# Optimization experiments

Measured on AMD Instinct MI355X. Metric: run time of the kernel, lower is better.

Reference implementation:

```python
import jax, jax.numpy as jnp
import numpy as np

N_NODES = 100000
N_EDGES = 1600000
IN_FEATS = 64
N_HIDDEN = 64
OUT_FEATS = 64


def setup_inputs() -> dict:
    key = jax.random.key(0)
    ks = jax.random.split(key, 12)
    feat = jax.random.normal(ks[0], (N_NODES, IN_FEATS), dtype=jnp.float32)
    # per-node symmetric degree normalization coefficients (e.g. 1/sqrt(deg))
    norm_data = jax.random.uniform(ks[1], (N_NODES,), dtype=jnp.float32, minval=0.1, maxval=1.0)
    src = jax.random.randint(ks[2], (N_EDGES,), 0, N_NODES)
    dst = jax.random.randint(ks[3], (N_EDGES,), 0, N_NODES)
    s = 0.05
    return {
        "feat": feat,
        "norm_data": norm_data,
        "src": src,
        "dst": dst,
        "W0": jax.random.normal(ks[4], (IN_FEATS, N_HIDDEN), dtype=jnp.float32) * s,
        "b0": jnp.zeros((N_HIDDEN,), dtype=jnp.float32),
        "W1": jax.random.normal(ks[5], (N_HIDDEN, N_HIDDEN), dtype=jnp.float32) * s,
        "b1": jnp.zeros((N_HIDDEN,), dtype=jnp.float32),
        "W2": jax.random.normal(ks[6], (N_HIDDEN, OUT_FEATS), dtype=jnp.float32) * s,
        "b2": jnp.zeros((OUT_FEATS,), dtype=jnp.float32),
    }


def _graph_conv(h, norm, src, dst, W, b, activation):
    # DGL GraphConv, norm='both': scale by src norm, project, aggregate over
    # edges (gather at src, scatter-add at dst), scale by dst norm, add bias.
    h = h * norm[:, None]                 # [N, d_in]
    h = h @ W                             # project first (d_in <= d_out path)
    msgs = jnp.take(h, src, axis=0)       # [E, d_out] irregular gather
    agg = jax.ops.segment_sum(msgs, dst, num_segments=N_NODES)  # [N, d_out]
    h = agg * norm[:, None] + b
    return jax.nn.relu(h) if activation else h


def reference(feat, norm_data, src, dst, W0, b0, W1, b1, W2, b2):
    h = _graph_conv(feat, norm_data, src, dst, W0, b0, True)
    h = _graph_conv(h, norm_data, src, dst, W1, b1, True)
    h = _graph_conv(h, norm_data, src, dst, W2, b2, False)
    return h
```

## Files before the change

kernel.cpp:

```cpp
#include <hip/hip_runtime.h>

#define FEATS 64
#define BTILE 32
#define MAX_NB 3200
#define CH 8192
#define SORT_CAP 2048
#define NPW 8

__device__ __forceinline__ float bf2f(unsigned short b) {
    unsigned u = (unsigned)b << 16;
    float f; __builtin_memcpy(&f, &u, 4); return f;
}
__device__ __forceinline__ unsigned short f2bf(float f) {
    unsigned u; __builtin_memcpy(&u, &f, 4);
    u += 0x7FFFu + ((u >> 16) & 1u);
    return (unsigned short)(u >> 16);
}
__device__ __forceinline__ float lo16(unsigned u) {
    unsigned v = u << 16; float f; __builtin_memcpy(&f, &v, 4); return f;
}
__device__ __forceinline__ float hi16(unsigned u) {
    unsigned v = u & 0xFFFF0000u; float f; __builtin_memcpy(&f, &v, 4); return f;
}

__global__ __launch_bounds__(256) void scale_kernel(
    const float* __restrict__ feat, const float* __restrict__ norm,
    unsigned short* __restrict__ out, int n4) {
    const int i = blockIdx.x * 256 + threadIdx.x;
    if (i >= n4) return;
    float4 v = reinterpret_cast<const float4*>(feat)[i];
    const float nv = norm[i >> 4];
    uint2 p;
    p.x = (unsigned)f2bf(v.x * nv) | ((unsigned)f2bf(v.y * nv) << 16);
    p.y = (unsigned)f2bf(v.z * nv) | ((unsigned)f2bf(v.w * nv) << 16);
    reinterpret_cast<uint2*>(out)[i] = p;
}

__global__ __launch_bounds__(1024) void hist_pass(
    const int* __restrict__ dst, int* __restrict__ hist, int E, int NB) {
    __shared__ int lh[MAX_NB];
    for (int i = threadIdx.x; i < NB; i += 1024) lh[i] = 0;
    __syncthreads();
    const int k  = blockIdx.x;
    const int e0 = k * CH, e1 = min(E, e0 + CH);
    for (int e = e0 + threadIdx.x; e < e1; e += 1024)
        atomicAdd(&lh[dst[e] >> 5], 1);
    __syncthreads();
    for (int b = threadIdx.x; b < NB; b += 1024)
        hist[(size_t)k * NB + b] = lh[b];
}

__global__ __launch_bounds__(256) void bucket_scan(
    int* hist, int* __restrict__ btotal, int NB, int NCHUNK) {
    __shared__ int sa[256], sb[256];
    const int b = blockIdx.x, t = threadIdx.x;
    const int v = (t < NCHUNK) ? hist[(size_t)t * NB + b] : 0;
    sa[t] = v;
    __syncthreads();
    int *cur = sa, *nxt = sb;
    for (int off = 1; off < 256; off <<= 1) {
        nxt[t] = cur[t] + ((t >= off) ? cur[t - off] : 0);
        __syncthreads();
        int* tmp = cur; cur = nxt; nxt = tmp;
    }
    if (t < NCHUNK) hist[(size_t)t * NB + b] = cur[t] - v;
    if (t == 255) btotal[b] = cur[255];
}

__global__ __launch_bounds__(1024) void base_scan(
    const int* __restrict__ btotal, int* __restrict__ bstart, int NB, int E) {
    __shared__ int sa[1024], sb[1024];
    __shared__ int carry;
    const int t = threadIdx.x;
    if (t == 0) carry = 0;
    __syncthreads();
    for (int base = 0; base < NB; base += 1024) {
        const int i = base + t;
        const int v = (i < NB) ? btotal[i] : 0;
        sa[t] = v;
        __syncthreads();
        int *cur = sa, *nxt = sb;
        for (int off = 1; off < 1024; off <<= 1) {
            nxt[t] = cur[t] + ((t >= off) ? cur[t - off] : 0);
            __syncthreads();
            int* tmp = cur; cur = nxt; nxt = tmp;
        }
        const int c = carry;
        if (i < NB) bstart[i] = c + cur[t] - v;
        __syncthreads();
        if (t == 1023) carry = c + cur[1023];
        __syncthreads();
    }
    if (t == 0) bstart[NB] = E;
}

__global__ __launch_bounds__(1024) void scatter_pack(
    const int* __restrict__ src, const int* __restrict__ dst,
    const int* __restrict__ prebase, const int* __restrict__ bstart,
    unsigned int* __restrict__ packed, int E, int NB) {
    __shared__ int cur[MAX_NB];
    const int k = blockIdx.x;
    for (int b = threadIdx.x; b < NB; b += 1024)
        cur[b] = bstart[b] + prebase[(size_t)k * NB + b];
    __syncthreads();
    const int e0 = k * CH, e1 = min(E, e0 + CH);
    for (int e = e0 + threadIdx.x; e < e1; e += 1024) {
        const int d = dst[e];
        const int p = atomicAdd(&cur[d >> 5], 1);
        packed[p] = ((unsigned)(d & 31) << 26) | (unsigned)src[e];
    }
}

__global__ __launch_bounds__(256) void sort_bucket(
    unsigned int* packed, const int* __restrict__ bstart,
    int* __restrict__ rowptr, int NB, int E) {
    __shared__ unsigned ent[SORT_CAP];
    __shared__ int cnt[BTILE];
    __shared__ int base[BTILE];
    const int b = blockIdx.x;
    const int beg = bstart[b], end = bstart[b + 1];
    const int n = end - beg;
    const int t = threadIdx.x;
    if (t < BTILE) cnt[t] = 0;
    __syncthreads();
    if (n <= SORT_CAP) {
        for (int i = t; i < n; i += 256) {
            const unsigned v = packed[beg + i];
            ent[i] = v;
            atomicAdd(&cnt[v >> 26], 1);
        }
    } else {
        for (int i = t; i < n; i += 256) atomicAdd(&cnt[packed[beg + i] >> 26], 1);
    }
    __syncthreads();
    if (t == 0) {
        int run = 0;
        for (int i = 0; i < BTILE; ++i) {
            const int c = cnt[i]; base[i] = run; cnt[i] = run; run += c;
        }
    }
    __syncthreads();
    if (t < BTILE) rowptr[b * BTILE + t] = beg + base[t];
    if (b == NB - 1 && t == 0) rowptr[NB * BTILE] = E;
    if (n <= SORT_CAP) {
        for (int i = t; i < n; i += 256) {
            const unsigned v = ent[i];
            const int p = atomicAdd(&cnt[v >> 26], 1);
            packed[beg + p] = v;
        }
    }
}

#define ACC8(d, m) do { \
    a0 = fmaf(lo16((d).x), (m), a0); a1 = fmaf(hi16((d).x), (m), a1); \
    a2 = fmaf(lo16((d).y), (m), a2); a3 = fmaf(hi16((d).y), (m), a3); \
    a4 = fmaf(lo16((d).z), (m), a4); a5 = fmaf(hi16((d).z), (m), a5); \
    a6 = fmaf(lo16((d).w), (m), a6); a7 = fmaf(hi16((d).w), (m), a7); } while (0)

#define RED(off) do { \
    a0 += __shfl_xor(a0, off, 64); a1 += __shfl_xor(a1, off, 64); \
    a2 += __shfl_xor(a2, off, 64); a3 += __shfl_xor(a3, off, 64); \
    a4 += __shfl_xor(a4, off, 64); a5 += __shfl_xor(a5, off, 64); \
    a6 += __shfl_xor(a6, off, 64); a7 += __shfl_xor(a7, off, 64); } while (0)

__device__ __forceinline__ uint4 row16(const unsigned short* hs, unsigned pk, int chunk) {
    return *((const uint4*)((const char*)hs + (size_t)(pk & 0x3FFFFFFu) * 128) + chunk);
}

__global__ __launch_bounds__(64, 4) void agg_proj(
    const unsigned int* __restrict__ packed, const int* __restrict__ rowptr,
    const unsigned short* __restrict__ hs, const float* __restrict__ norm,
    const float* __restrict__ W, const float* __restrict__ bias,
    void* __restrict__ outv, int N, int E, int mode) {
    __shared__ float accs[NPW * FEATS];
    const int lane  = threadIdx.x & 63;
    const int slot  = lane >> 3;
    const int chunk = lane & 7;
    const int node0 = blockIdx.x * NPW;

    int rbv[NPW], rev[NPW];
    unsigned c[NPW];
#pragma unroll
    for (int i = 0; i < NPW; ++i) {
        const int node = node0 + i;
        const int cl = node < N ? node : N - 1;
        rbv[i] = rowptr[cl];
        rev[i] = (node < N) ? rowptr[cl + 1] : rbv[i];
        c[i]   = packed[min(rbv[i] + lane, E - 1)];
    }

#pragma unroll
    for (int i = 0; i < NPW; ++i) {
        float a0 = 0.f, a1 = 0.f, a2 = 0.f, a3 = 0.f,
              a4 = 0.f, a5 = 0.f, a6 = 0.f, a7 = 0.f;
        const int deg = rev[i] - rbv[i];
        if (deg > 0) {
            const int segn = min(deg, 64);
            const int no   = (segn + 7) >> 3;
            unsigned pk = (unsigned)__builtin_amdgcn_ds_bpermute(slot << 2, (int)c[i]);
            uint4 d = row16(hs, pk, chunk);
            float m = (slot < segn) ? 1.f : 0.f;
            for (int o = 1; o < no; ++o) {
                const int idx = o * 8 + slot;
                unsigned pk1 = (unsigned)__builtin_amdgcn_ds_bpermute(idx << 2, (int)c[i]);
                uint4 d1 = row16(hs, pk1, chunk);
                ACC8(d, m);
                d = d1; m = (idx < segn) ? 1.f : 0.f;
            }
            ACC8(d, m);
            for (int p = rbv[i] + 64; p < rev[i]; p += 64) {
                const int sn = min(rev[i] - p, 64);
                const unsigned cw2 = packed[min(p + lane, E - 1)];
                const int no2 = (sn + 7) >> 3;
                for (int o = 0; o < no2; ++o) {
                    const int idx = o * 8 + slot;
                    unsigned pk2 = (unsigned)__builtin_amdgcn_ds_bpermute(idx << 2, (int)cw2);
                    uint4 d2 = row16(hs, pk2, chunk);
                    const float m2 = (idx < sn) ? 1.f : 0.f;
                    ACC8(d2, m2);
                }
            }
        }
        RED(8); RED(16); RED(32);
        if (slot == 0) {
            float4* dstp = (float4*)&accs[i * FEATS + chunk * 8];
            dstp[0] = make_float4(a0, a1, a2, a3);
            dstp[1] = make_float4(a4, a5, a6, a7);
        }
    }
    __syncthreads();

    float s[NPW];
#pragma unroll
    for (int i = 0; i < NPW; ++i) s[i] = 0.f;
#pragma unroll 1
    for (int k4 = 0; k4 < 16; ++k4) {
        const float w0 = W[(4 * k4 + 0) * FEATS + lane];
        const float w1 = W[(4 * k4 + 1) * FEATS + lane];
        const float w2 = W[(4 * k4 + 2) * FEATS + lane];
        const float w3 = W[(4 * k4 + 3) * FEATS + lane];
#pragma unroll
        for (int i = 0; i < NPW; ++i) {
            const float4 a = *(const float4*)&accs[i * FEATS + 4 * k4];
            s[i] = fmaf(a.w, w3, fmaf(a.z, w2, fmaf(a.y, w1, fmaf(a.x, w0, s[i]))));
        }
    }
    const float bi = bias[lane];
#pragma unroll
    for (int i = 0; i < NPW; ++i) {
        const int node = node0 + i;
        if (node >= N) break;
        const float nv = norm[node];
        float o = fmaf(s[i], nv, bi);
        if (mode) {
            o = fmaxf(o, 0.f) * nv;
            ((unsigned short*)outv)[(size_t)node * FEATS + lane] = f2bf(o);
        } else {
            ((float*)outv)[(size_t)node * FEATS + lane] = o;
        }
    }
}

extern "C" void kernel_launch(void* const* d_in, const int* in_sizes, int n_in,
                              void* d_out, int out_size, void* d_ws, size_t ws_size,
                              hipStream_t stream) {
    const float* feat = (const float*)d_in[0];
    const float* norm = (const float*)d_in[1];
    const int*   src  = (const int*)d_in[2];
    const int*   dst  = (const int*)d_in[3];
    const float* W0   = (const float*)d_in[4];
    const float* b0   = (const float*)d_in[5];
    const float* W1   = (const float*)d_in[6];
    const float* b1   = (const float*)d_in[7];
    const float* W2   = (const float*)d_in[8];
    const float* b2   = (const float*)d_in[9];

    float* out = (float*)d_out;
    const int N = in_sizes[0] / FEATS;
    const int E = in_sizes[2];
    const int NB = (N + BTILE - 1) / BTILE;
    const int NCHUNK = (E + CH - 1) / CH;

    unsigned short* H0 = (unsigned short*)d_ws;
    unsigned short* H1 = H0 + (size_t)N * FEATS;
    unsigned* packed = (unsigned*)(H1 + (size_t)N * FEATS);
    int*      hist   = (int*)(packed + E);
    int*      btotal = hist + (size_t)NCHUNK * NB;
    int*      bstart = btotal + NB;
    int*      rowptr = bstart + NB + 1;

    hist_pass<<<NCHUNK, 1024, 0, stream>>>(dst, hist, E, NB);
    bucket_scan<<<NB, 256, 0, stream>>>(hist, btotal, NB, NCHUNK);
    base_scan<<<1, 1024, 0, stream>>>(btotal, bstart, NB, E);
    scatter_pack<<<NCHUNK, 1024, 0, stream>>>(src, dst, hist, bstart, packed, E, NB);
    sort_bucket<<<NB, 256, 0, stream>>>(packed, bstart, rowptr, NB, E);

    const int agrid = (N + NPW - 1) / NPW;
    const int sgrid = (N * 16 + 255) / 256;

    scale_kernel<<<sgrid, 256, 0, stream>>>(feat, norm, H0, N * 16);

    agg_proj<<<agrid, 64, 0, stream>>>(packed, rowptr, H0, norm, W0, b0, H1, N, E, 1);
    agg_proj<<<agrid, 64, 0, stream>>>(packed, rowptr, H1, norm, W1, b1, H0, N, E, 1);
    agg_proj<<<agrid, 64, 0, stream>>>(packed, rowptr, H0, norm, W2, b2, out, N, E, 0);
}
```

Measured before the change: 221.0 us.

## Assign each 8-lane group to one node instead of whole wave per node

Restructures the aggregation so each group of 8 lanes owns one destination node and walks its neighbour list sequentially, instead of the whole 64-lane wave cooperatively gathering one node's edges and reducing across lanes with shuffles. This removes the bpermute broadcasts, the masked FMAs and the cross-lane shuffle reductions, and gives per-node parallelism across the eight nodes in a block. In exchange, each lane group serially loads one packed index per edge with a short prefetch, so latency hiding per node is lower and degree imbalance among the eight nodes causes divergence within the wave.

```diff
diff --git a/kernel.cpp b/kernel.cpp
--- a/kernel.cpp
+++ b/kernel.cpp
@@ -151,17 +151,11 @@
     }
 }
 
-#define ACC8(d, m) do { \
-    a0 = fmaf(lo16((d).x), (m), a0); a1 = fmaf(hi16((d).x), (m), a1); \
-    a2 = fmaf(lo16((d).y), (m), a2); a3 = fmaf(hi16((d).y), (m), a3); \
-    a4 = fmaf(lo16((d).z), (m), a4); a5 = fmaf(hi16((d).z), (m), a5); \
-    a6 = fmaf(lo16((d).w), (m), a6); a7 = fmaf(hi16((d).w), (m), a7); } while (0)
-
-#define RED(off) do { \
-    a0 += __shfl_xor(a0, off, 64); a1 += __shfl_xor(a1, off, 64); \
-    a2 += __shfl_xor(a2, off, 64); a3 += __shfl_xor(a3, off, 64); \
-    a4 += __shfl_xor(a4, off, 64); a5 += __shfl_xor(a5, off, 64); \
-    a6 += __shfl_xor(a6, off, 64); a7 += __shfl_xor(a7, off, 64); } while (0)
+#define ADD8(d) do { \
+    a0 += lo16((d).x); a1 += hi16((d).x); \
+    a2 += lo16((d).y); a3 += hi16((d).y); \
+    a4 += lo16((d).z); a5 += hi16((d).z); \
+    a6 += lo16((d).w); a7 += hi16((d).w); } while (0)
 
 __device__ __forceinline__ uint4 row16(const unsigned short* hs, unsigned pk, int chunk) {
     return *((const uint4*)((const char*)hs + (size_t)(pk & 0x3FFFFFFu) * 128) + chunk);
@@ -177,56 +171,31 @@
     const int slot  = lane >> 3;
     const int chunk = lane & 7;
     const int node0 = blockIdx.x * NPW;
-
-    int rbv[NPW], rev[NPW];
-    unsigned c[NPW];
-#pragma unroll
-    for (int i = 0; i < NPW; ++i) {
-        const int node = node0 + i;
-        const int cl = node < N ? node : N - 1;
-        rbv[i] = rowptr[cl];
-        rev[i] = (node < N) ? rowptr[cl + 1] : rbv[i];
-        c[i]   = packed[min(rbv[i] + lane, E - 1)];
-    }
-
-#pragma unroll
-    for (int i = 0; i < NPW; ++i) {
-        float a0 = 0.f, a1 = 0.f, a2 = 0.f, a3 = 0.f,
-              a4 = 0.f, a5 = 0.f, a6 = 0.f, a7 = 0.f;
-        const int deg = rev[i] - rbv[i];
-        if (deg > 0) {
-            const int segn = min(deg, 64);
-            const int no   = (segn + 7) >> 3;
-            unsigned pk = (unsigned)__builtin_amdgcn_ds_bpermute(slot << 2, (int)c[i]);
-            uint4 d = row16(hs, pk, chunk);
-            float m = (slot < segn) ? 1.f : 0.f;
-            for (int o = 1; o < no; ++o) {
-                const int idx = o * 8 + slot;
-                unsigned pk1 = (unsigned)__builtin_amdgcn_ds_bpermute(idx << 2, (int)c[i]);
-                uint4 d1 = row16(hs, pk1, chunk);
-                ACC8(d, m);
-                d = d1; m = (idx < segn) ? 1.f : 0.f;
-            }
-            ACC8(d, m);
-            for (int p = rbv[i] + 64; p < rev[i]; p += 64) {
-                const int sn = min(rev[i] - p, 64);
-                const unsigned cw2 = packed[min(p + lane, E - 1)];
-                const int no2 = (sn + 7) >> 3;
-                for (int o = 0; o < no2; ++o) {
-                    const int idx = o * 8 + slot;
-                    unsigned pk2 = (unsigned)__builtin_amdgcn_ds_bpermute(idx << 2, (int)cw2);
-                    uint4 d2 = row16(hs, pk2, chunk);
-                    const float m2 = (idx < sn) ? 1.f : 0.f;
-                    ACC8(d2, m2);
-                }
-            }
-        }
-        RED(8); RED(16); RED(32);
-        if (slot == 0) {
-            float4* dstp = (float4*)&accs[i * FEATS + chunk * 8];
-            dstp[0] = make_float4(a0, a1, a2, a3);
-            dstp[1] = make_float4(a4, a5, a6, a7);
-        }
+    const int node  = node0 + slot;
+
+    float a0 = 0.f, a1 = 0.f, a2 = 0.f, a3 = 0.f,
+          a4 = 0.f, a5 = 0.f, a6 = 0.f, a7 = 0.f;
+
+    int rb = 0, deg = 0;
+    if (node < N) { rb = rowptr[node]; deg = rowptr[node + 1] - rb; }
+
+    if (deg > 0) {
+        unsigned pk0 = packed[rb];
+        unsigned pk1 = packed[rb + min(1, deg - 1)];
+        uint4 d0 = row16(hs, pk0, chunk);
+        for (int j = 1; j < deg; ++j) {
+            const unsigned pk2 = packed[rb + min(j + 1, deg - 1)];
+            const uint4 d1 = row16(hs, pk1, chunk);
+            ADD8(d0);
+            d0 = d1; pk1 = pk2;
+        }
+        ADD8(d0);
+    }
+
+    {
+        float4* dstp = (float4*)&accs[slot * FEATS + chunk * 8];
+        dstp[0] = make_float4(a0, a1, a2, a3);
+        dstp[1] = make_float4(a4, a5, a6, a7);
     }
     __syncthreads();
 
@@ -248,15 +217,15 @@
     const float bi = bias[lane];
 #pragma unroll
     for (int i = 0; i < NPW; ++i) {
-        const int node = node0 + i;
-        if (node >= N) break;
-        const float nv = norm[node];
+        const int onode = node0 + i;
+        if (onode >= N) break;
+        const float nv = norm[onode];
         float o = fmaf(s[i], nv, bi);
         if (mode) {
             o = fmaxf(o, 0.f) * nv;
-            ((unsigned short*)outv)[(size_t)node * FEATS + lane] = f2bf(o);
+            ((unsigned short*)outv)[(size_t)onode * FEATS + lane] = f2bf(o);
         } else {
-            ((float*)outv)[(size_t)node * FEATS + lane] = o;
+            ((float*)outv)[(size_t)onode * FEATS + lane] = o;
         }
     }
 }
```

Result: faster. 190.1 us (median of 2 runs) (-14.0%).
